# Kernel optimization log

Hardware: AMD Instinct MI355X
Metric: run time of the kernel (lower is better)

## Reference

```python
import jax, jax.numpy as jnp
import numpy as np

N = 50000   # nodes
E = 800000  # edges (avg degree 16)
D = 128     # in_hidden == out_hidden
BN_EPS = 1e-5


def prelu(x, a):
    return jnp.where(x >= 0, x, a * x)


def setup_inputs() -> dict:
    key = jax.random.key(0)
    ks = jax.random.split(key, 6)
    feat = jax.random.normal(ks[0], (N, D), dtype=jnp.float32)
    src = jax.random.randint(ks[1], (E,), 0, N, dtype=jnp.int32)
    dst = jax.random.randint(ks[2], (E,), 0, N, dtype=jnp.int32)
    W = jax.random.normal(ks[3], (D, D), dtype=jnp.float32) / np.float32(np.sqrt(D))
    b = jnp.zeros((D,), jnp.float32)
    a1 = jnp.full((1,), 0.25, jnp.float32)   # PReLU inside GraphConv
    gamma = jnp.ones((D,), jnp.float32)      # BatchNorm weight
    beta = jnp.zeros((D,), jnp.float32)      # BatchNorm bias
    a2 = jnp.full((1,), 0.25, jnp.float32)   # outer PReLU
    return {"feat": feat, "src": src, "dst": dst, "W": W, "b": b,
            "a1": a1, "gamma": gamma, "beta": beta, "a2": a2}


def reference(feat, src, dst, W, b, a1, gamma, beta, a2):
    ones = jnp.ones((E,), jnp.float32)
    # degree normalization (norm='both'), degrees clamped to >= 1 as in DGL
    deg_out = jnp.clip(jax.ops.segment_sum(ones, src, num_segments=N), 1.0)
    deg_in = jnp.clip(jax.ops.segment_sum(ones, dst, num_segments=N), 1.0)
    norm_src = deg_out ** -0.5  # [N]
    norm_dst = deg_in ** -0.5   # [N]

    # dropout is identity at inference
    x = feat * norm_src[:, None]                                   # [N, D]
    agg = jax.ops.segment_sum(x[src], dst, num_segments=N)          # gather-scatter SpMM
    h = (agg @ W) * norm_dst[:, None] + b                           # [N, D]
    h = prelu(h, a1)                                                # GraphConv activation

    # BatchNorm1d (training-mode batch stats, biased variance)
    mean = jnp.mean(h, axis=0)
    var = jnp.mean((h - mean) ** 2, axis=0)
    h = (h - mean) * jax.lax.rsqrt(var + BN_EPS) * gamma + beta

    return prelu(h, a2)
```

## Files before the change

kernel.cpp:

```cpp
#include <hip/hip_runtime.h>
#include <math.h>

#define DD 128
#define EBCAP 4608
#define ELLC 64
#define APB 3200
typedef unsigned int uint32;
typedef unsigned short u16;
typedef __attribute__((ext_vector_type(8))) short bf16x8;
typedef __attribute__((ext_vector_type(4))) float f32x4;

__device__ __forceinline__ u16 f2bf(float x) {
    unsigned u = __float_as_uint(x);
    unsigned r = (u + 0x7FFFu + ((u >> 16) & 1u)) >> 16;
    return (u16)r;
}

__device__ __forceinline__ float bflo(uint32 v) { return __uint_as_float(v << 16); }
__device__ __forceinline__ float bfhi(uint32 v) { return __uint_as_float(v & 0xFFFF0000u); }

__global__ __launch_bounds__(256) void binsort_kernel(
    const int* __restrict__ src, const int* __restrict__ dst,
    int* __restrict__ gcntD, int* __restrict__ gcntS,
    uint32* __restrict__ gbinD, u16* __restrict__ gbinS, int E) {
    __shared__ int hD[256], scD[256], cuD[256], baseD[256];
    __shared__ int hS[256], scS[256], cuS[256], baseS[256];
    __shared__ uint32 st[APB], sd[APB], ss[APB];

    int tid = threadIdx.x;
    int e0 = blockIdx.x * APB;
    int cnt = E - e0; if (cnt > APB) cnt = APB; if (cnt < 0) cnt = 0;

    hD[tid] = 0; hS[tid] = 0;
    __syncthreads();

    for (int j = tid; j < cnt; j += 256) {
        int s = src[e0 + j], d = dst[e0 + j];
        int bD = d >> 8, bS = s >> 8;
        st[j] = ((uint32)bD << 24) | ((uint32)(d & 255) << 16) | (uint32)s;
        atomicAdd(&hD[bD], 1);
        atomicAdd(&hS[bS], 1);
    }
    __syncthreads();

    cuD[tid] = hD[tid]; cuS[tid] = hS[tid];
    __syncthreads();
    for (int off = 1; off < 256; off <<= 1) {
        int vD = cuD[tid], vS = cuS[tid];
        int aD = (tid >= off) ? cuD[tid - off] : 0;
        int aS = (tid >= off) ? cuS[tid - off] : 0;
        __syncthreads();
        cuD[tid] = vD + aD; cuS[tid] = vS + aS;
        __syncthreads();
    }
    scD[tid] = cuD[tid] - hD[tid];
    scS[tid] = cuS[tid] - hS[tid];
    cuD[tid] = scD[tid];
    cuS[tid] = scS[tid];
    baseD[tid] = 0; baseS[tid] = 0;
    if (hD[tid] > 0) baseD[tid] = atomicAdd(&gcntD[tid], hD[tid]);
    if (hS[tid] > 0) baseS[tid] = atomicAdd(&gcntS[tid], hS[tid]);
    __syncthreads();

    for (int j = tid; j < cnt; j += 256) {
        uint32 e = st[j];
        int bD = e >> 24;
        sd[atomicAdd(&cuD[bD], 1)] = e;
        int s = e & 0xFFFF, bS = s >> 8;
        ss[atomicAdd(&cuS[bS], 1)] = ((uint32)bS << 16) | (uint32)s;
    }
    __syncthreads();

    for (int j = tid; j < cnt; j += 256) {
        uint32 e = sd[j];
        int bD = e >> 24;
        int pos = baseD[bD] + (j - scD[bD]);
        if (pos < EBCAP) gbinD[bD * EBCAP + pos] = e;
        uint32 f = ss[j];
        int bS = f >> 16;
        int pos2 = baseS[bS] + (j - scS[bS]);
        if (pos2 < EBCAP) gbinS[bS * EBCAP + pos2] = (u16)f;
    }
}

__global__ __launch_bounds__(256) void binbuild_kernel(
    const uint32* __restrict__ gbinD, const int* __restrict__ gcntD,
    u16* __restrict__ gell, int* __restrict__ degI, float* __restrict__ normI, int N) {
    int b = blockIdx.x, tid = threadIdx.x;
    __shared__ int cn[256], cu[256];
    __shared__ u16 ell[256 * ELLC];

    int cnt = min(gcntD[b], EBCAP);
    cn[tid] = 0;
    __syncthreads();
    const uint32* bp = gbinD + (long long)b * EBCAP;
    for (int j = tid; j < cnt; j += 256)
        atomicAdd(&cn[(bp[j] >> 16) & 255], 1);
    __syncthreads();

    int node = b * 256 + tid;
    if (node < N) {
        int d = cn[tid];
        degI[node] = min(d, ELLC);
        normI[node] = rsqrtf(fmaxf((float)d, 1.0f));
    }
    cu[tid] = 0;
    __syncthreads();

    for (int j = tid; j < cnt; j += 256) {
        uint32 e = bp[j];
        int n = (e >> 16) & 255;
        int r = atomicAdd(&cu[n], 1);
        if (r < ELLC) ell[n * ELLC + r] = (u16)e;
    }
    __syncthreads();

    uint32* eu = (uint32*)ell;
    uint32* go = (uint32*)(gell + (long long)b * 256 * ELLC);
    for (int k = tid; k < 256 * ELLC / 2; k += 256) go[k] = eu[k];
}

__global__ __launch_bounds__(256) void srccnt_kernel(
    const u16* __restrict__ gbinS, const int* __restrict__ gcntS,
    float* __restrict__ normO, int N) {
    int b = blockIdx.x, tid = threadIdx.x;
    __shared__ int cn[256];
    int cnt = min(gcntS[b], EBCAP);
    cn[tid] = 0;
    __syncthreads();
    const u16* bp = gbinS + (long long)b * EBCAP;
    for (int j = tid; j < cnt; j += 256)
        atomicAdd(&cn[bp[j] & 255], 1);
    __syncthreads();
    int node = b * 256 + tid;
    if (node < N) normO[node] = rsqrtf(fmaxf((float)cn[tid], 1.0f));
}

__global__ __launch_bounds__(256) void wtk_kernel(
    const float* __restrict__ W, u16* __restrict__ wt) {
    int idx = blockIdx.x * 256 + threadIdx.x;
    int col = idx >> 7, k = idx & 127;
    wt[idx] = f2bf(W[k * DD + col]);
}

__global__ __launch_bounds__(256) void gemm_kernel(
    const float* __restrict__ feat, const u16* __restrict__ wt,
    const float* __restrict__ normO, u16* __restrict__ ybf, int N) {
    __shared__ u16 Xs[DD * DD];
    __shared__ u16 Ws[DD * DD];
    int tid = threadIdx.x;
    int r0g = blockIdx.x * 128;

    const uint32* wt32 = (const uint32*)wt;
#pragma unroll
    for (int it = 0; it < 32; ++it) {
        int e32 = it * 256 + tid;
        uint32 v = wt32[e32];
        int col = e32 >> 6;
        int byte = (e32 * 4) ^ ((col & 7) << 4);
        *(uint32*)((char*)Ws + byte) = v;
    }

    const float4* F4 = (const float4*)feat;
#pragma unroll
    for (int it = 0; it < 16; ++it) {
        int e4 = it * 256 + tid;
        int row = e4 >> 5;
        int k0 = (e4 & 31) * 4;
        int grow = min(r0g + row, N - 1);
        float sc = normO[grow];
        float4 v = F4[(long long)grow * 32 + (e4 & 31)];
        uint32 lo = (uint32)f2bf(v.x * sc) | ((uint32)f2bf(v.y * sc) << 16);
        uint32 hi = (uint32)f2bf(v.z * sc) | ((uint32)f2bf(v.w * sc) << 16);
        int byte = (row * 256 + k0 * 2) ^ ((row & 7) << 4);
        *(uint2*)((char*)Xs + byte) = make_uint2(lo, hi);
    }
    __syncthreads();

    int lane = tid & 63;
    int w = tid >> 6;
    int lr = lane & 15, lg = lane >> 4;
    int rowb = w * 32;

    bf16x8 a[2][4];
#pragma unroll
    for (int rt = 0; rt < 2; ++rt)
#pragma unroll
        for (int kk = 0; kk < 4; ++kk) {
            int row = rowb + rt * 16 + lr;
            int byte = (row * 256 + (kk * 32 + lg * 8) * 2) ^ ((row & 7) << 4);
            a[rt][kk] = *(bf16x8*)((char*)Xs + byte);
        }

    f32x4 acc[2][8];
#pragma unroll
    for (int rt = 0; rt < 2; ++rt)
#pragma unroll
        for (int ct = 0; ct < 8; ++ct)
            acc[rt][ct] = (f32x4){0.f, 0.f, 0.f, 0.f};

#pragma unroll
    for (int ct = 0; ct < 8; ++ct) {
        bf16x8 b[4];
        int col = ct * 16 + lr;
#pragma unroll
        for (int kk = 0; kk < 4; ++kk) {
            int byte = (col * 256 + (kk * 32 + lg * 8) * 2) ^ ((col & 7) << 4);
            b[kk] = *(bf16x8*)((char*)Ws + byte);
        }
#pragma unroll
        for (int rt = 0; rt < 2; ++rt)
#pragma unroll
            for (int kk = 0; kk < 4; ++kk)
                acc[rt][ct] = __builtin_amdgcn_mfma_f32_16x16x32_bf16(
                    a[rt][kk], b[kk], acc[rt][ct], 0, 0, 0);
    }

#pragma unroll
    for (int rt = 0; rt < 2; ++rt)
#pragma unroll
        for (int ct = 0; ct < 8; ++ct)
#pragma unroll
            for (int reg = 0; reg < 4; ++reg) {
                int row = r0g + rowb + rt * 16 + lg * 4 + reg;
                if (row < N)
                    ybf[(long long)row * DD + ct * 16 + lr] = f2bf(acc[rt][ct][reg]);
            }
}

__global__ __launch_bounds__(256) void gather_kernel(
    const uint32* __restrict__ ybf, const u16* __restrict__ gell,
    const int* __restrict__ degI, const float* __restrict__ normI,
    const float* __restrict__ bias, const float* __restrict__ a1p,
    float* __restrict__ out, int N) {
    __shared__ u16 sidx[16 * ELLC];
    __shared__ int sdeg[16];
    __shared__ float snrm[16];

    int tid = threadIdx.x;
    int nb = blockIdx.x * 16;

    const uint32* g = (const uint32*)(gell + (long long)nb * ELLC);
    uint32* si = (uint32*)sidx;
#pragma unroll
    for (int k = 0; k < 2; ++k) si[tid + k * 256] = g[tid + k * 256];
    if (tid < 16) {
        int node = nb + tid;
        sdeg[tid] = (node < N) ? degI[node] : 0;
        snrm[tid] = (node < N) ? normI[node] : 1.0f;
    }
    __syncthreads();

    int slot = tid >> 4;
    int c4 = tid & 15;
    int node = nb + slot;
    int deg = sdeg[slot];
    const u16* my = sidx + slot * ELLC;
    const uint4* y4 = (const uint4*)ybf;

    float a0 = 0.f, a1 = 0.f, a2 = 0.f, a3 = 0.f;
    float a4 = 0.f, a5 = 0.f, a6 = 0.f, a7 = 0.f;

    int j = 0;
    for (; j + 2 <= deg; j += 2) {
        int s0 = my[j], s1 = my[j + 1];
        uint4 v0 = y4[(long long)s0 * 16 + c4];
        uint4 v1 = y4[(long long)s1 * 16 + c4];
        a0 += bflo(v0.x); a1 += bfhi(v0.x);
        a2 += bflo(v0.y); a3 += bfhi(v0.y);
        a4 += bflo(v0.z); a5 += bfhi(v0.z);
        a6 += bflo(v0.w); a7 += bfhi(v0.w);
        a0 += bflo(v1.x); a1 += bfhi(v1.x);
        a2 += bflo(v1.y); a3 += bfhi(v1.y);
        a4 += bflo(v1.z); a5 += bfhi(v1.z);
        a6 += bflo(v1.w); a7 += bfhi(v1.w);
    }
    if (j < deg) {
        uint4 v0 = y4[(long long)my[j] * 16 + c4];
        a0 += bflo(v0.x); a1 += bfhi(v0.x);
        a2 += bflo(v0.y); a3 += bfhi(v0.y);
        a4 += bflo(v0.z); a5 += bfhi(v0.z);
        a6 += bflo(v0.w); a7 += bfhi(v0.w);
    }

    if (node >= N) return;
    float nd = snrm[slot];
    float alpha = *a1p;
    const float4* b4 = (const float4*)bias;
    float4 b0 = b4[c4 * 2], b1 = b4[c4 * 2 + 1];
    float4 o0, o1;
    o0.x = a0 * nd + b0.x; o0.y = a1 * nd + b0.y;
    o0.z = a2 * nd + b0.z; o0.w = a3 * nd + b0.w;
    o1.x = a4 * nd + b1.x; o1.y = a5 * nd + b1.y;
    o1.z = a6 * nd + b1.z; o1.w = a7 * nd + b1.w;
    o0.x = o0.x >= 0.f ? o0.x : alpha * o0.x;
    o0.y = o0.y >= 0.f ? o0.y : alpha * o0.y;
    o0.z = o0.z >= 0.f ? o0.z : alpha * o0.z;
    o0.w = o0.w >= 0.f ? o0.w : alpha * o0.w;
    o1.x = o1.x >= 0.f ? o1.x : alpha * o1.x;
    o1.y = o1.y >= 0.f ? o1.y : alpha * o1.y;
    o1.z = o1.z >= 0.f ? o1.z : alpha * o1.z;
    o1.w = o1.w >= 0.f ? o1.w : alpha * o1.w;
    float4* o4 = (float4*)out;
    o4[(long long)node * 32 + c4 * 2] = o0;
    o4[(long long)node * 32 + c4 * 2 + 1] = o1;
}

__global__ __launch_bounds__(256) void stats_kernel(
    const float* __restrict__ h, float* __restrict__ stats, int N) {
    int tid = threadIdx.x;
    long long idx = (long long)blockIdx.x * 256 + tid;
    long long stride = (long long)gridDim.x * 256;
    long long total = (long long)N * DD;
    float s = 0.0f, s2 = 0.0f;
    for (long long i = idx; i < total; i += stride) {
        float v = h[i];
        s += v;
        s2 += v * v;
    }
    __shared__ float ls[256], lq[256];
    ls[tid] = s;
    lq[tid] = s2;
    __syncthreads();
    if (tid < DD) {
        atomicAdd(&stats[tid], ls[tid] + ls[tid + DD]);
        atomicAdd(&stats[DD + tid], lq[tid] + lq[tid + DD]);
    }
}

__global__ void bnparam_kernel(const float* __restrict__ stats,
                               const float* __restrict__ gamma, const float* __restrict__ beta,
                               float* __restrict__ sA, float* __restrict__ sB, float invN) {
    int c = threadIdx.x;
    if (c < DD) {
        float mean = stats[c] * invN;
        float ex2 = stats[DD + c] * invN;
        float var = ex2 - mean * mean;
        float inv = rsqrtf(var + 1e-5f);
        float g = gamma[c] * inv;
        sA[c] = g;
        sB[c] = beta[c] - mean * g;
    }
}

__global__ __launch_bounds__(256) void final_kernel(
    float* __restrict__ h, const float* __restrict__ sA, const float* __restrict__ sB,
    const float* __restrict__ a2p, int total4) {
    int i = blockIdx.x * 256 + threadIdx.x;
    if (i >= total4) return;
    float alpha = *a2p;
    int c4 = i & (DD / 4 - 1);
    float4 v = ((float4*)h)[i];
    float4 a = ((const float4*)sA)[c4];
    float4 b = ((const float4*)sB)[c4];
    float4 o;
    o.x = v.x * a.x + b.x;
    o.y = v.y * a.y + b.y;
    o.z = v.z * a.z + b.z;
    o.w = v.w * a.w + b.w;
    o.x = o.x >= 0.0f ? o.x : alpha * o.x;
    o.y = o.y >= 0.0f ? o.y : alpha * o.y;
    o.z = o.z >= 0.0f ? o.z : alpha * o.z;
    o.w = o.w >= 0.0f ? o.w : alpha * o.w;
    ((float4*)h)[i] = o;
}

extern "C" void kernel_launch(void* const* d_in, const int* in_sizes, int n_in,
                              void* d_out, int out_size, void* d_ws, size_t ws_size,
                              hipStream_t stream) {
    const float* feat  = (const float*)d_in[0];
    const int*   src   = (const int*)d_in[1];
    const int*   dst   = (const int*)d_in[2];
    const float* W     = (const float*)d_in[3];
    const float* bias  = (const float*)d_in[4];
    const float* a1    = (const float*)d_in[5];
    const float* gamma = (const float*)d_in[6];
    const float* beta  = (const float*)d_in[7];
    const float* a2    = (const float*)d_in[8];
    float* out = (float*)d_out;

    int N = in_sizes[0] / DD;
    int E = in_sizes[1];
    int nbins = (N + 255) >> 8;

    long long off = 0;
    int* gcntD = (int*)d_ws;                         off += 256;
    int* gcntS = (int*)d_ws + off;                   off += 256;
    float* stats = (float*)((int*)d_ws + off);       off += 512;
    int* degI = (int*)d_ws + off;                    off += N;
    float* normI = (float*)((int*)d_ws + off);       off += N;
    float* normO = (float*)((int*)d_ws + off);       off += N;
    u16* wt = (u16*)((uint32*)d_ws + off);           off += 8192;
    uint32* gbinD = (uint32*)d_ws + off;             off += (long long)nbins * EBCAP;
    u16* gbinS = (u16*)((uint32*)d_ws + off);        off += (long long)nbins * EBCAP / 2;
    u16* gell = (u16*)((uint32*)d_ws + off);         off += (long long)nbins * 256 * ELLC / 2;
    uint32* ybf = (uint32*)d_ws + off;

    hipMemsetAsync(d_ws, 0, 1024 * sizeof(int), stream);

    int gridA = (E + APB - 1) / APB;
    binsort_kernel<<<gridA, 256, 0, stream>>>(src, dst, gcntD, gcntS, gbinD, gbinS, E);
    binbuild_kernel<<<nbins, 256, 0, stream>>>(gbinD, gcntD, gell, degI, normI, N);
    srccnt_kernel<<<nbins, 256, 0, stream>>>(gbinS, gcntS, normO, N);

    wtk_kernel<<<64, 256, 0, stream>>>(W, wt);

    int gridG = (N + 127) / 128;
    gemm_kernel<<<gridG, 256, 0, stream>>>(feat, wt, normO, (u16*)ybf, N);

    int gather_blocks = (N + 15) / 16;
    gather_kernel<<<gather_blocks, 256, 0, stream>>>(ybf, gell, degI, normI, bias, a1, out, N);

    stats_kernel<<<512, 256, 0, stream>>>(out, stats, N);
    bnparam_kernel<<<1, 128, 0, stream>>>(stats, gamma, beta, stats + 256, stats + 384, 1.0f / (float)N);

    int total4 = N * DD / 4;
    final_kernel<<<(total4 + 255) / 256, 256, 0, stream>>>(out, stats + 256, stats + 384, a2, total4);
}
```

Baseline: 127.2 us.

## Fuse BatchNorm statistics into gather kernel with per-block partials and reduction

The gather kernel now computes per-column sums and sums of squares of its outputs through wave shuffles and shared memory, and writes per-block partials. A separate reduce kernel then sums them deterministically. This replaces the stats kernel, which re-read the full 25.6 MB output. The memset is also replaced by a small zero kernel. The cost is extra shuffles, shared memory and a block barrier in gather, plus a partial buffer of about 3 MB and its reduction.

```diff
diff --git a/kernel.cpp b/kernel.cpp
--- a/kernel.cpp
+++ b/kernel.cpp
@@ -18,6 +18,11 @@
 
 __device__ __forceinline__ float bflo(uint32 v) { return __uint_as_float(v << 16); }
 __device__ __forceinline__ float bfhi(uint32 v) { return __uint_as_float(v & 0xFFFF0000u); }
+
+__global__ void zero_kernel(int4* __restrict__ p) {
+    int i = threadIdx.x;
+    if (i < 128) p[i] = make_int4(0, 0, 0, 0);
+}
 
 __global__ __launch_bounds__(256) void binsort_kernel(
     const int* __restrict__ src, const int* __restrict__ dst,
@@ -232,10 +237,11 @@
     const uint32* __restrict__ ybf, const u16* __restrict__ gell,
     const int* __restrict__ degI, const float* __restrict__ normI,
     const float* __restrict__ bias, const float* __restrict__ a1p,
-    float* __restrict__ out, int N) {
+    float* __restrict__ out, float* __restrict__ partial, int N) {
     __shared__ u16 sidx[16 * ELLC];
     __shared__ int sdeg[16];
     __shared__ float snrm[16];
+    __shared__ float lsum[4][128], lsq[4][128];
 
     int tid = threadIdx.x;
     int nb = blockIdx.x * 16;
@@ -254,6 +260,7 @@
     int slot = tid >> 4;
     int c4 = tid & 15;
     int node = nb + slot;
+    bool valid = node < N;
     int deg = sdeg[slot];
     const u16* my = sidx + slot * ELLC;
     const uint4* y4 = (const uint4*)ybf;
@@ -283,7 +290,6 @@
         a6 += bflo(v0.w); a7 += bfhi(v0.w);
     }
 
-    if (node >= N) return;
     float nd = snrm[slot];
     float alpha = *a1p;
     const float4* b4 = (const float4*)bias;
@@ -301,31 +307,54 @@
     o1.y = o1.y >= 0.f ? o1.y : alpha * o1.y;
     o1.z = o1.z >= 0.f ? o1.z : alpha * o1.z;
     o1.w = o1.w >= 0.f ? o1.w : alpha * o1.w;
-    float4* o4 = (float4*)out;
-    o4[(long long)node * 32 + c4 * 2] = o0;
-    o4[(long long)node * 32 + c4 * 2 + 1] = o1;
-}
-
-__global__ __launch_bounds__(256) void stats_kernel(
-    const float* __restrict__ h, float* __restrict__ stats, int N) {
+
+    if (valid) {
+        float4* o4 = (float4*)out;
+        o4[(long long)node * 32 + c4 * 2] = o0;
+        o4[(long long)node * 32 + c4 * 2 + 1] = o1;
+    }
+
+    float v[8] = {o0.x, o0.y, o0.z, o0.w, o1.x, o1.y, o1.z, o1.w};
+    float s[8], q[8];
+#pragma unroll
+    for (int k = 0; k < 8; ++k) {
+        float x = valid ? v[k] : 0.f;
+        s[k] = x; q[k] = x * x;
+    }
+#pragma unroll
+    for (int k = 0; k < 8; ++k) {
+        s[k] += __shfl_xor(s[k], 16, 64); q[k] += __shfl_xor(q[k], 16, 64);
+        s[k] += __shfl_xor(s[k], 32, 64); q[k] += __shfl_xor(q[k], 32, 64);
+    }
+    int wv = tid >> 6, lane = tid & 63;
+    if (lane < 16) {
+#pragma unroll
+        for (int k = 0; k < 8; ++k) {
+            lsum[wv][lane * 8 + k] = s[k];
+            lsq[wv][lane * 8 + k] = q[k];
+        }
+    }
+    __syncthreads();
+    if (tid < 128) {
+        float ps = lsum[0][tid] + lsum[1][tid] + lsum[2][tid] + lsum[3][tid];
+        float pq = lsq[0][tid] + lsq[1][tid] + lsq[2][tid] + lsq[3][tid];
+        partial[(long long)blockIdx.x * 256 + tid] = ps;
+        partial[(long long)blockIdx.x * 256 + 128 + tid] = pq;
+    }
+}
+
+__global__ __launch_bounds__(256) void reduce_kernel(
+    const float* __restrict__ partial, float* __restrict__ stats, int nblocks) {
+    int col = blockIdx.x;
     int tid = threadIdx.x;
-    long long idx = (long long)blockIdx.x * 256 + tid;
-    long long stride = (long long)gridDim.x * 256;
-    long long total = (long long)N * DD;
-    float s = 0.0f, s2 = 0.0f;
-    for (long long i = idx; i < total; i += stride) {
-        float v = h[i];
-        s += v;
-        s2 += v * v;
-    }
-    __shared__ float ls[256], lq[256];
-    ls[tid] = s;
-    lq[tid] = s2;
-    __syncthreads();
-    if (tid < DD) {
-        atomicAdd(&stats[tid], ls[tid] + ls[tid + DD]);
-        atomicAdd(&stats[DD + tid], lq[tid] + lq[tid + DD]);
-    }
+    float s = 0.f;
+    for (int r = tid; r < nblocks; r += 256)
+        s += partial[(long long)r * 256 + col];
+    for (int off = 32; off; off >>= 1) s += __shfl_down(s, off, 64);
+    __shared__ float ws[4];
+    if ((tid & 63) == 0) ws[tid >> 6] = s;
+    __syncthreads();
+    if (tid == 0) stats[col] = ws[0] + ws[1] + ws[2] + ws[3];
 }
 
 __global__ void bnparam_kernel(const float* __restrict__ stats,
@@ -382,6 +411,7 @@
     int N = in_sizes[0] / DD;
     int E = in_sizes[1];
     int nbins = (N + 255) >> 8;
+    int gblocks = (N + 15) / 16;
 
     long long off = 0;
     int* gcntD = (int*)d_ws;                         off += 256;
@@ -391,12 +421,13 @@
     float* normI = (float*)((int*)d_ws + off);       off += N;
     float* normO = (float*)((int*)d_ws + off);       off += N;
     u16* wt = (u16*)((uint32*)d_ws + off);           off += 8192;
+    float* partial = (float*)((uint32*)d_ws + off);  off += (long long)gblocks * 256;
     uint32* gbinD = (uint32*)d_ws + off;             off += (long long)nbins * EBCAP;
     u16* gbinS = (u16*)((uint32*)d_ws + off);        off += (long long)nbins * EBCAP / 2;
     u16* gell = (u16*)((uint32*)d_ws + off);         off += (long long)nbins * 256 * ELLC / 2;
     uint32* ybf = (uint32*)d_ws + off;
 
-    hipMemsetAsync(d_ws, 0, 1024 * sizeof(int), stream);
+    zero_kernel<<<1, 128, 0, stream>>>((int4*)d_ws);
 
     int gridA = (E + APB - 1) / APB;
     binsort_kernel<<<gridA, 256, 0, stream>>>(src, dst, gcntD, gcntS, gbinD, gbinS, E);
@@ -408,10 +439,9 @@
     int gridG = (N + 127) / 128;
     gemm_kernel<<<gridG, 256, 0, stream>>>(feat, wt, normO, (u16*)ybf, N);
 
-    int gather_blocks = (N + 15) / 16;
-    gather_kernel<<<gather_blocks, 256, 0, stream>>>(ybf, gell, degI, normI, bias, a1, out, N);
-
-    stats_kernel<<<512, 256, 0, stream>>>(out, stats, N);
+    gather_kernel<<<gblocks, 256, 0, stream>>>(ybf, gell, degI, normI, bias, a1, out, partial, N);
+
+    reduce_kernel<<<256, 256, 0, stream>>>(partial, stats, gblocks);
     bnparam_kernel<<<1, 128, 0, stream>>>(stats, gamma, beta, stats + 256, stats + 384, 1.0f / (float)N);
 
     int total4 = N * DD / 4;
```

After: 109.6 us. 1.16x faster.
